# Performance work log

Hardware: AMD Instinct MI355X
Metric: run time of the kernel (lower is better)

The kernel has to match this reference:

```python
import jax, jax.numpy as jnp
import numpy as np

FS = 44100.0
TWO_PI = 2.0 * np.pi


def setup_inputs() -> dict:
    key = jax.random.key(0)
    ks = jax.random.split(key, 12)
    B, T, H, NF, NB = 4, 64000, 96, 4, 8
    f0 = jax.random.uniform(ks[0], (B, T, 1), minval=100.0, maxval=400.0)
    amplitudes = jax.random.uniform(ks[1], (B, T, H))
    vibrato_rate = 5.0 + jax.random.uniform(ks[2], (B, T, 1))
    vibrato_depth = 0.2 * jax.random.uniform(ks[3], (B, T, 1))
    ff = jnp.array([800.0, 1150.0, 2900.0, 3900.0], dtype=jnp.float32)
    fb = jnp.array([80.0, 90.0, 120.0, 130.0], dtype=jnp.float32)
    fg = jnp.array([1.0, 0.5, 0.25, 0.1], dtype=jnp.float32)
    formant_freqs = ff[None, None] * (0.9 + 0.2 * jax.random.uniform(ks[4], (B, T, NF)))
    formant_bandwidths = fb[None, None] * (0.9 + 0.2 * jax.random.uniform(ks[5], (B, T, NF)))
    formant_gains = fg[None, None] * (0.9 + 0.2 * jax.random.uniform(ks[6], (B, T, NF)))
    glottal_open_quotient = 0.5 + 0.4 * jax.random.uniform(ks[7], (B, T, 1))
    phase_coherence = jax.random.uniform(ks[8], (B, T, 1))
    breathiness = 0.3 * jax.random.uniform(ks[9], (B, T, 1))
    breath_spectral_shape = jax.random.uniform(ks[10], (B, T, NB))
    initial_phase = jnp.zeros((B, 1, 1), dtype=jnp.float32)
    return dict(f0=f0, amplitudes=amplitudes, vibrato_rate=vibrato_rate,
                vibrato_depth=vibrato_depth, formant_freqs=formant_freqs,
                formant_bandwidths=formant_bandwidths, formant_gains=formant_gains,
                glottal_open_quotient=glottal_open_quotient,
                phase_coherence=phase_coherence, breathiness=breathiness,
                breath_spectral_shape=breath_spectral_shape, initial_phase=initial_phase)


def _breath_noise(noise, spectral_weights):
    # noise: [B,T]; spectral_weights: [B,n_bands] (mid frame) -> normalized shaped noise [B,T]
    B, T = noise.shape
    n_bands = spectral_weights.shape[1]
    shaped = jnp.zeros_like(noise)
    for i in range(n_bands):  # small fixed band loop (structurally distinct kernel sizes)
        smooth = 2.0 ** (i / 2.0)
        ksz = max(3, int(128 / smooth))
        if ksz % 2 == 0:
            ksz += 1
        g = np.exp(-np.arange(-(ksz // 2), ksz // 2 + 1) ** 2 / (2.0 * (ksz / 6.0) ** 2))
        kern = jnp.asarray(g / g.sum(), dtype=jnp.float32)
        smoothed = jax.lax.conv_general_dilated(
            noise[:, None, :], kern[None, None, :], (1,), 'SAME')[:, 0, :]
        shaped = shaped + smoothed * spectral_weights[:, i:i + 1]
    mean = shaped.mean(axis=1, keepdims=True)
    std = shaped.std(axis=1, ddof=1, keepdims=True) + 1e-8
    return (shaped - mean) / std


def _forward(f0, amplitudes, vibrato_rate, vibrato_depth, formant_freqs,
             formant_bandwidths, formant_gains, glottal_open_quotient,
             phase_coherence, breathiness, breath_spectral_shape, initial_phase, noise):
    B, T, H = amplitudes.shape
    fs = FS
    # --- vibrato ---
    t = (jnp.arange(T, dtype=jnp.float32) / fs)[None, :, None]
    vib_factor = 2.0 ** (vibrato_depth / 12.0)
    vib_mult = jnp.exp(jnp.sin(TWO_PI * vibrato_rate * t) * jnp.log(vib_factor))
    f0_vib = jnp.where(f0 > 0, f0 * vib_mult, f0)  # B,T,1
    # --- per-harmonic phases via cumulative fundamental phase ---
    fund_phase = jnp.cumsum(TWO_PI * f0_vib / fs, axis=1) + initial_phase  # B,T,1
    n = jnp.arange(1, H + 1, dtype=jnp.float32)  # harmonic numbers
    phases = fund_phase * n  # B,T,H
    # --- phase coherence: blend higher harmonics toward n * fundamental ---
    coherent = fund_phase * n[1:]
    blended = phase_coherence * coherent + (1.0 - phase_coherence) * phases[:, :, 1:]
    phases = jnp.concatenate([phases[:, :, :1], blended], axis=2)
    # --- remove above Nyquist ---
    amp = jnp.where(f0_vib * n < fs / 2.0, amplitudes, jnp.zeros_like(amplitudes))
    # --- glottal flow model ---
    norm_phase = jnp.mod(phases, TWO_PI) / TWO_PI
    oq = glottal_open_quotient
    half_pi = jnp.float32(np.pi / 2.0)
    rising = jnp.sin(norm_phase / oq * half_pi) ** 2
    falling = jnp.cos((norm_phase - oq) / (1.0 - oq) * half_pi) ** 2
    flow = jnp.where(norm_phase < oq, rising, falling) - 0.5
    signal = jnp.sum(flow * amp, axis=-1)  # B,T
    # --- formant filter (mid-frame params, vectorized over batch & formants) ---
    mid = T // 2
    freqs = jnp.fft.rfftfreq(T, d=1.0 / fs).astype(jnp.float32)  # [F]
    fmid = formant_freqs[:, mid][:, :, None]       # B,NF,1
    bwmid = formant_bandwidths[:, mid][:, :, None]
    gmid = formant_gains[:, mid][:, :, None]
    resp = (gmid / (1.0 + ((freqs[None, None, :] - fmid) / (bwmid / 2.0)) ** 2)).sum(1)  # B,F
    filtered = jnp.fft.irfft(jnp.fft.rfft(signal) * resp, n=T)  # B,T
    # --- breath noise mix ---
    breath = _breath_noise(noise, breath_spectral_shape[:, mid])  # B,T
    br = breathiness[:, :, 0]
    out = filtered * (1.0 - br) + breath * br
    final_phase = jnp.mod(fund_phase[:, -1:, :], TWO_PI)  # B,1,1
    return out, final_phase


def reference(f0, amplitudes, vibrato_rate, vibrato_depth, formant_freqs,
              formant_bandwidths, formant_gains, glottal_open_quotient,
              phase_coherence, breathiness, breath_spectral_shape, initial_phase):
    B, T = f0.shape[0], f0.shape[1]
    noise = jax.random.normal(jax.random.key(42), (B, T), dtype=jnp.float32)
    return _forward(f0, amplitudes, vibrato_rate, vibrato_depth, formant_freqs,
                    formant_bandwidths, formant_gains, glottal_open_quotient,
                    phase_coherence, breathiness, breath_spectral_shape,
                    initial_phase, noise)
```

## Files before the change

kernel.cpp:

```cpp
#include <hip/hip_runtime.h>
#include <math.h>
#include <stdint.h>

#define B_ 4
#define T_ 64000
#define H_ 96
#define NCH 1000
#define TT_ 64
#define TWO_PI_D 6.283185307179586

typedef float2 cplx;
__device__ __forceinline__ cplx cadd(cplx a, cplx b){ return make_float2(a.x+b.x, a.y+b.y); }
__device__ __forceinline__ cplx csub(cplx a, cplx b){ return make_float2(a.x-b.x, a.y-b.y); }
__device__ __forceinline__ cplx cmul(cplx a, cplx b){ return make_float2(a.x*b.x - a.y*b.y, a.x*b.y + a.y*b.x); }

__device__ float  g_dpf[B_*T_];
__device__ unsigned char g_hcnt[B_*T_];
__device__ float  g_signal[B_*T_];
__device__ float  g_shaped[B_*T_];
__device__ float  g_Kcomb[B_][132];
__device__ float2 g_W1[2*512*125];
__device__ float2 g_Z[2*125*512];
__device__ double g_chunksum[B_*NCH];
__device__ double g_stats[B_*2];
__device__ double g_part[B_*250*2];

__device__ __forceinline__ double fsin64(double x){
  double z = x * 0.63661977236758138243;
  double fn = floor(z + 0.5);
  int k = (int)fn;
  const double p1 = 1.57079632673412561417e+00;
  const double p2 = 6.07710050650619224932e-11;
  double r = x - fn*p1;
  r = r - fn*p2;
  double s = r*r;
  double ps = 1.58969099521155010221e-10;
  ps = ps*s - 2.50507602534068634195e-08;
  ps = ps*s + 2.75573137070700676789e-06;
  ps = ps*s - 1.98412698298579493134e-04;
  ps = ps*s + 8.33333333332248946124e-03;
  ps = ps*s - 1.66666666666666324348e-01;
  double sr = r + r*s*ps;
  double pc = -1.13596475577881948265e-11;
  pc = pc*s + 2.08757232129817482790e-09;
  pc = pc*s - 2.75573143513906633035e-07;
  pc = pc*s + 2.48015872894767294178e-05;
  pc = pc*s - 1.38888888888741095749e-03;
  pc = pc*s + 4.16666666666666019037e-02;
  double cr = 1.0 - 0.5*s + s*s*pc;
  int m = k & 3;
  return (m==0) ? sr : (m==1) ? cr : (m==2) ? -sr : -cr;
}

__device__ __forceinline__ double fexp_small(double x){
  double p = 1.9841269841269841e-04;
  p = p*x + 1.3888888888888889e-03;
  p = p*x + 8.3333333333333332e-03;
  p = p*x + 4.1666666666666664e-02;
  p = p*x + 1.6666666666666666e-01;
  p = p*x + 0.5;
  p = p*x + 1.0;
  p = p*x + 1.0;
  return p;
}

__device__ __forceinline__ uint32_t rotl32(uint32_t x, int r){ return (x<<r)|(x>>(32-r)); }

__device__ __forceinline__ uint32_t threefry_bits(uint32_t i){
  uint32_t x0 = 0u, x1 = i;
  const uint32_t ks0 = 0u, ks1 = 42u, ks2 = 0u ^ 42u ^ 0x1BD11BDAu;
  x0 += ks0; x1 += ks1;
  #define TFR(r) { x0 += x1; x1 = rotl32(x1, r); x1 ^= x0; }
  TFR(13) TFR(15) TFR(26) TFR(6)   x0 += ks1; x1 += ks2 + 1u;
  TFR(17) TFR(29) TFR(16) TFR(24)  x0 += ks2; x1 += ks0 + 2u;
  TFR(13) TFR(15) TFR(26) TFR(6)   x0 += ks0; x1 += ks1 + 3u;
  TFR(17) TFR(29) TFR(16) TFR(24)  x0 += ks1; x1 += ks2 + 4u;
  TFR(13) TFR(15) TFR(26) TFR(6)   x0 += ks2; x1 += ks0 + 5u;
  #undef TFR
  return x0 ^ x1;
}

__device__ __forceinline__ float bits_to_normal(uint32_t bits){
  uint32_t mbits = (bits >> 9) | 0x3F800000u;
  float f = __uint_as_float(mbits) - 1.0f;
  const float lo = -0.99999994f;
  float x = f * 2.0f + lo;
  x = fmaxf(lo, x);
  float w = -log1pf(-x*x);
  float p;
  if (w < 5.0f){
    w -= 2.5f;
    p = 2.81022636e-08f;
    p = fmaf(p, w, 3.43273939e-07f);
    p = fmaf(p, w, -3.5233877e-06f);
    p = fmaf(p, w, -4.39150654e-06f);
    p = fmaf(p, w, 0.00021858087f);
    p = fmaf(p, w, -0.00125372503f);
    p = fmaf(p, w, -0.00417768164f);
    p = fmaf(p, w, 0.246640727f);
    p = fmaf(p, w, 1.50140941f);
  } else {
    w = sqrtf(w) - 3.0f;
    p = -0.000200214257f;
    p = fmaf(p, w, 0.000100950558f);
    p = fmaf(p, w, 0.00134934322f);
    p = fmaf(p, w, -0.00367342844f);
    p = fmaf(p, w, 0.00573950773f);
    p = fmaf(p, w, -0.0076224613f);
    p = fmaf(p, w, 0.00943887047f);
    p = fmaf(p, w, 1.00167406f);
    p = fmaf(p, w, 2.83297682f);
  }
  return 1.4142135623730951f * (p * x);
}

__constant__ int KSZc[8] = {129,91,65,45,33,23,17,11};

__global__ __launch_bounds__(256) void k_phase(const float* __restrict__ bss,
                                               const float* __restrict__ f0,
                                               const float* __restrict__ vr,
                                               const float* __restrict__ vd){
  int b = blockIdx.x / 250, c = blockIdx.x % 250;
  int t0 = c*256, tid = threadIdx.x;
  if (c == 0){
    __shared__ float wn[8];
    {
      int i = tid >> 5, l32 = tid & 31;
      int ksz = KSZc[i];
      float sig = (float)ksz / 6.0f;
      float inv2s2 = 1.0f/(2.0f*sig*sig);
      int ctr = ksz>>1;
      float s = 0.f;
      for (int j = l32; j < ksz; j += 32){
        float d = (float)(j - ctr);
        s += expf(-d*d*inv2s2);
      }
      #pragma unroll
      for (int o=1;o<32;o<<=1) s += __shfl_xor(s, o);
      if (l32 == 0) wn[i] = bss[((size_t)b*T_ + T_/2)*8 + i] / s;
    }
    __syncthreads();
    if (tid < 129){
      int tau = tid - 64;
      float acc = 0.f;
      #pragma unroll
      for (int i=0;i<8;i++){
        int ksz = KSZc[i]; int hw = ksz>>1;
        if (tau >= -hw && tau <= hw){
          float sig = (float)ksz/6.0f;
          float inv2s2 = 1.0f/(2.0f*sig*sig);
          acc += expf(-(float)(tau*tau)*inv2s2) * wn[i];
        }
      }
      g_Kcomb[b][tid] = acc;
    }
  }
  int t = t0 + tid;
  int idx = b*T_ + t;
  double tt = (double)t * 2.2675736961451248e-05;
  double argd = TWO_PI_D * (double)vr[idx] * tt;
  double argr = argd - TWO_PI_D * floor(argd * 0.15915494309189535);
  float svf = __sinf((float)argr);
  double lm = (double)vd[idx] * 0.057762265046662105;
  double vm = fexp_small((double)svf * lm);
  double f0s = (double)f0[idx];
  double f0v = (f0s > 0.0) ? f0s * vm : f0s;
  int cnt;
  if (f0v <= 0.0) cnt = 96;
  else {
    int n = (int)(22050.0f / (float)f0v);
    if (!((double)n * f0v < 22050.0)) n--;
    if ((double)(n+1) * f0v < 22050.0) n++;
    double dlo = 22050.0 - (double)n * f0v;
    double dhi = (double)(n+1) * f0v - 22050.0;
    if (dlo < 0.01 || dhi < 0.01){
      double sv_d = fsin64(argd);
      double vm_d = fexp_small(sv_d * lm);
      double f0x = f0s * vm_d;
      int n2 = (int)(22050.0f / (float)f0x);
      if (!((double)n2 * f0x < 22050.0)) n2--;
      if ((double)(n2+1) * f0x < 22050.0) n2++;
      n = n2;
      f0v = f0x;
    }
    cnt = (n < 0) ? 0 : ((n > 96) ? 96 : n);
  }
  g_hcnt[idx] = (unsigned char)cnt;
  double v = f0v * 1.4247585730565955e-04;
  g_dpf[idx] = (float)v;
  int lane = tid & 63, wid = tid >> 6;
  for (int o=1;o<64;o<<=1) v += __shfl_down(v, o);
  if (lane == 0) g_chunksum[b*NCH + c*4 + wid] = v;
}

__global__ __launch_bounds__(256) void k_synth(const float* __restrict__ amps,
                                               const float* __restrict__ goq,
                                               const float* __restrict__ iph,
                                               float* __restrict__ out_final){
  __shared__ float sh_ns[384];
  __shared__ float sh_kl[132];
  __shared__ float sh_ph[TT_];
  __shared__ double sh_red[8];
  int bid = blockIdx.x;
  int tid = threadIdx.x;
  if ((bid % 5) == 4){
    int bb = bid / 5;
    int b = bb / 250, c = bb % 250;
    int t0 = c * 256;
    for (int k = tid; k < 384; k += 256){
      int t = t0 - 64 + k;
      float nv = 0.f;
      if (t >= 0 && t < T_) nv = bits_to_normal(threefry_bits((uint32_t)(b*T_ + t)));
      sh_ns[k] = nv;
    }
    for (int k = tid; k < 129; k += 256) sh_kl[k] = g_Kcomb[b][k];
    __syncthreads();
    float acc = 0.f;
    for (int j = 0; j < 129; j++) acc = fmaf(sh_ns[tid + j], sh_kl[j], acc);
    g_shaped[b*T_ + t0 + tid] = acc;
    double xx = (double)acc;
    double s1 = xx, s2 = xx*xx;
    for (int o=1;o<64;o<<=1){ s1 += __shfl_down(s1,o); s2 += __shfl_down(s2,o); }
    int lane = tid&63, wid = tid>>6;
    if (lane==0){ sh_red[wid] = s1; sh_red[4+wid] = s2; }
    __syncthreads();
    if (tid==0){
      g_part[(b*250+c)*2]   = sh_red[0]+sh_red[1]+sh_red[2]+sh_red[3];
      g_part[(b*250+c)*2+1] = sh_red[4]+sh_red[5]+sh_red[6]+sh_red[7];
    }
  } else {
    int sb = bid - bid/5;
    int b = sb / NCH, c = sb % NCH;
    int t0 = c * TT_;
    int tl = tid >> 2, part = tid & 3;
    const float4* Ar = (const float4*)(amps + ((size_t)b*T_ + t0 + tl)*H_ + part*24);
    float4 a0 = Ar[0], a1 = Ar[1], a2 = Ar[2], a3 = Ar[3], a4 = Ar[4], a5 = Ar[5];
    int idx = b*T_ + t0 + tl;
    int hc = (int)g_hcnt[idx];
    float oq = goq[idx];
    if (tid < 64){
      double s = 0.0;
      for (int ch = tid; ch < c; ch += 64) s += g_chunksum[b*NCH + ch];
      for (int o=1;o<64;o<<=1) s += __shfl_xor(s, o);
      double base = s + (double)iph[b];
      int idq = b*T_ + t0 + tid;
      double v = (double)g_dpf[idq];
      for (int o=1;o<64;o<<=1){ double u = __shfl_up(v, o); if (tid >= o) v += u; }
      sh_ph[tid] = (float)fmod(base + v, TWO_PI_D);
      if (c == NCH-1 && tid == 63) out_final[b] = (float)fmod(base + v, TWO_PI_D);
    }
    __syncthreads();
    float r = sh_ph[tl];
    float k1 = 3.14159265358979f / oq;
    float k2 = 3.14159265358979f / (1.0f - oq);
    float offA = 3.14159265358979f;
    float offB = -oq * k2;
    float r0 = r * 0.15915494309189535f;
    int hbase = part*24;
    float sum = 0.f;
    float av[24] = {a0.x,a0.y,a0.z,a0.w, a1.x,a1.y,a1.z,a1.w, a2.x,a2.y,a2.z,a2.w,
                    a3.x,a3.y,a3.z,a3.w, a4.x,a4.y,a4.z,a4.w, a5.x,a5.y,a5.z,a5.w};
    #pragma unroll
    for (int e=0;e<24;e++){
      int h = hbase + e;
      float amp = (h < hc) ? av[e] : 0.0f;
      float nn = (float)(h+1);
      float fr = nn * r0;
      fr = fr - floorf(fr);
      bool ris = fr < oq;
      float kk  = ris ? k1 : k2;
      float off = ris ? offA : offB;
      float cv = __cosf(fmaf(fr, kk, off));
      sum = fmaf(cv, amp, sum);
    }
    sum += __shfl_xor(sum, 1);
    sum += __shfl_xor(sum, 2);
    if (part == 0) g_signal[idx] = 0.5f * sum;
  }
}

template<int SGN>
__device__ __forceinline__ float2* fft512_r4(float2* bufA, float2* bufB, int tid){
  float2* src = bufA; float2* dst = bufB;
  #pragma unroll
  for (int st=0; st<4; st++){
    const int s = 1<<(2*st);
    const int n = 512>>(2*st);
    const int m = n>>2;
    if (tid < 128){
      int p = tid / s;
      int q = tid - p*s;
      float2 a0 = src[q + s*p];
      float2 a1 = src[q + s*(p+m)];
      float2 a2 = src[q + s*(p+2*m)];
      float2 a3 = src[q + s*(p+3*m)];
      float2 t0 = cadd(a0,a2), t1 = csub(a0,a2);
      float2 t2 = cadd(a1,a3), t3 = csub(a1,a3);
      float2 it3 = make_float2(-(float)SGN*t3.y, (float)SGN*t3.x);
      float2 r0 = cadd(t0,t2);
      float2 r1 = cadd(t1,it3);
      float2 r2 = csub(t0,t2);
      float2 r3 = csub(t1,it3);
      float ba = (float)SGN * ((float)(2.0*M_PI)/(float)n) * (float)p;
      dst[q + s*(4*p+0)] = r0;
      float sw,cw;
      __sincosf(ba, &sw, &cw);
      dst[q + s*(4*p+1)] = cmul(make_float2(cw,sw), r1);
      __sincosf(2.f*ba, &sw, &cw);
      dst[q + s*(4*p+2)] = cmul(make_float2(cw,sw), r2);
      __sincosf(3.f*ba, &sw, &cw);
      dst[q + s*(4*p+3)] = cmul(make_float2(cw,sw), r3);
    }
    __syncthreads();
    float2* tp = src; src = dst; dst = tp;
  }
  {
    float2 a = src[tid];
    float2 bb = src[tid+256];
    dst[tid]     = cadd(a,bb);
    dst[tid+256] = csub(a,bb);
    __syncthreads();
    float2* tp = src; src = dst; dst = tp;
  }
  return src;
}

__device__ __forceinline__ cplx w5k(int k, float sgn){
  const float C[5] = {1.f, 0.30901699f, -0.80901699f, -0.80901699f, 0.30901699f};
  const float S[5] = {0.f, 0.95105652f, 0.58778525f, -0.58778525f, -0.95105652f};
  return make_float2(C[k], sgn*S[k]);
}

template<int SGN>
__device__ __forceinline__ float2* fft125_rows(float2* bufA, float2* bufB, int tid){
  float2* src = bufA; float2* dst = bufB;
  #pragma unroll
  for (int st=0; st<3; st++){
    const int s = (st==0)?1:((st==1)?5:25);
    const int n = (st==0)?125:((st==1)?25:5);
    const int m = n/5;
    if (tid < 200){
      int row = tid/25, w = tid - row*25;
      int p = w/s, q = w - p*s;
      int base = row*125 + q;
      float2 a0 = src[base + s*p];
      float2 a1 = src[base + s*(p+m)];
      float2 a2 = src[base + s*(p+2*m)];
      float2 a3 = src[base + s*(p+3*m)];
      float2 a4 = src[base + s*(p+4*m)];
      #pragma unroll
      for (int r2=0;r2<5;r2++){
        float2 acc = a0;
        acc = cadd(acc, cmul(a1, w5k((1*r2)%5, (float)SGN)));
        acc = cadd(acc, cmul(a2, w5k((2*r2)%5, (float)SGN)));
        acc = cadd(acc, cmul(a3, w5k((3*r2)%5, (float)SGN)));
        acc = cadd(acc, cmul(a4, w5k((4*r2)%5, (float)SGN)));
        float ang = (float)SGN * ((float)(2.0*M_PI)/(float)n) * (float)(p*r2);
        float sw,cw; __sincosf(ang,&sw,&cw);
        dst[base + s*(5*p+r2)] = cmul(make_float2(cw,sw), acc);
      }
    }
    __syncthreads();
    float2* tp = src; src = dst; dst = tp;
  }
  return src;
}

__global__ __launch_bounds__(256) void k_fft512_fwd(){
  int p = blockIdx.x / 125, n1 = blockIdx.x % 125;
  int tid = threadIdx.x;
  __shared__ float2 bufA[512];
  __shared__ float2 bufB[512];
  const float* sa = g_signal + (size_t)(2*p)*T_;
  const float* sb = g_signal + (size_t)(2*p+1)*T_;
  for (int i=tid;i<512;i+=256) bufA[i] = make_float2(sa[n1 + 125*i], sb[n1 + 125*i]);
  __syncthreads();
  float2* res = fft512_r4<-1>(bufA, bufB, tid);
  for (int i=tid;i<512;i+=256){
    float ang = -(float)(2.0*M_PI/64000.0) * (float)(n1*i);
    float sw,cw; __sincosf(ang,&sw,&cw);
    g_W1[((size_t)p*512 + i)*125 + n1] = cmul(make_float2(cw,sw), res[i]);
  }
  if (blockIdx.x < B_){
    int b = blockIdx.x;
    double s1=0.0, s2=0.0;
    if (tid < 250){ s1 = g_part[(b*250+tid)*2]; s2 = g_part[(b*250+tid)*2+1]; }
    for (int o=1;o<64;o<<=1){ s1 += __shfl_down(s1,o); s2 += __shfl_down(s2,o); }
    __shared__ double a1[4], a2[4];
    int lane = tid&63, wid = tid>>6;
    if (lane==0){ a1[wid]=s1; a2[wid]=s2; }
    __syncthreads();
    if (tid==0){
      double S1=a1[0]+a1[1]+a1[2]+a1[3], S2=a2[0]+a2[1]+a2[2]+a2[3];
      double mean = S1 / (double)T_;
      double var = (S2 - (double)T_*mean*mean) / (double)(T_-1);
      if (var < 0.0) var = 0.0;
      double rstd = 1.0/(sqrt(var) + 1e-8);
      g_stats[b*2] = mean; g_stats[b*2+1] = rstd;
    }
  }
}

__global__ __launch_bounds__(256) void k_fft125_mid(const float* __restrict__ ffq,
                                                    const float* __restrict__ fbw,
                                                    const float* __restrict__ fgn){
  int p = blockIdx.x / 64;
  int j = blockIdx.x % 64;
  int tid = threadIdx.x;
  __shared__ float2 bufA[1000];
  __shared__ float2 bufB[1000];
  int k2r[8];
  #pragma unroll
  for (int l=0;l<8;l++){
    int k2;
    if (l < 4) k2 = 4*j + l;
    else if (j==0 && l==4) k2 = 256;
    else k2 = 512 - 4*j - (l-4);
    k2r[l] = k2;
  }
  for (int i=tid;i<1000;i+=256){
    int l = i/125, n1 = i - l*125;
    bufA[i] = g_W1[((size_t)p*512 + k2r[l])*125 + n1];
  }
  float fca[4], bwa[4], ga[4], fcb[4], bwb[4], gb[4];
  int ba = 2*p, bb = 2*p+1;
  #pragma unroll
  for (int q=0;q<4;q++){
    size_t ia = ((size_t)ba*T_ + T_/2)*4 + q;
    size_t ib = ((size_t)bb*T_ + T_/2)*4 + q;
    fca[q]=ffq[ia]; bwa[q]=fbw[ia]; ga[q]=fgn[ia];
    fcb[q]=ffq[ib]; bwb[q]=fbw[ib]; gb[q]=fgn[ib];
  }
  __syncthreads();
  float2* X = fft125_rows<-1>(bufA, bufB, tid);
  float2* Y = (X == bufA) ? bufB : bufA;
  for (int i=tid;i<1000;i+=256){
    int l = i/125, k1 = i - l*125;
    int k2 = k2r[l];
    int lm = ((j==0) && (l==0 || l==4)) ? l : (l^4);
    int k1m = (k2 == 0) ? ((k1==0)?0:(125-k1)) : (124-k1);
    float2 Z1 = X[l*125 + k1];
    float2 Z2 = X[lm*125 + k1m];
    float xax = 0.5f*(Z1.x + Z2.x), xay = 0.5f*(Z1.y - Z2.y);
    float xbx = 0.5f*(Z1.y + Z2.y), xby = -0.5f*(Z1.x - Z2.x);
    int f = k2 + 512*k1;
    int fi = (f <= 32000) ? f : (64000 - f);
    float freq = (float)fi * 0.6890625f;
    float ra = 0.f, rb = 0.f;
    #pragma unroll
    for (int q=0;q<4;q++){
      float da = (freq - fca[q]) / (bwa[q]*0.5f);
      ra += ga[q] / (1.0f + da*da);
      float db = (freq - fcb[q]) / (bwb[q]*0.5f);
      rb += gb[q] / (1.0f + db*db);
    }
    float yax = ra*xax, yay = ra*xay;
    float ybx = rb*xbx, yby = rb*xby;
    Y[i] = make_float2(yax - yby, yay + ybx);
  }
  __syncthreads();
  float2* res2 = fft125_rows<1>(Y, X, tid);
  for (int i=tid;i<1000;i+=256){
    int l = i/125, n1 = i - l*125;
    int k2 = k2r[l];
    float ang = (float)(2.0*M_PI/64000.0) * (float)(n1*k2);
    float sw,cw; __sincosf(ang,&sw,&cw);
    g_Z[((size_t)p*125 + n1)*512 + k2] = cmul(make_float2(cw,sw), res2[i]);
  }
}

__global__ __launch_bounds__(256) void k_fft512_inv(const float* __restrict__ brth,
                                                    float* __restrict__ outp){
  int p = blockIdx.x / 125, n1 = blockIdx.x % 125;
  int tid = threadIdx.x;
  __shared__ float2 bufA[512];
  __shared__ float2 bufB[512];
  const float2* gin = g_Z + ((size_t)p*125 + n1)*512;
  for (int i=tid;i<512;i+=256) bufA[i] = gin[i];
  __syncthreads();
  float2* res = fft512_r4<1>(bufA, bufB, tid);
  int ba = 2*p, bb = 2*p+1;
  float mean_a = (float)g_stats[ba*2], rstd_a = (float)g_stats[ba*2+1];
  float mean_b = (float)g_stats[bb*2], rstd_b = (float)g_stats[bb*2+1];
  for (int i=tid;i<512;i+=256){
    int t = n1 + 125*i;
    float2 v = res[i];
    {
      int idx = ba*T_ + t;
      float filt = v.x * (1.0f/64000.0f);
      float br = brth[idx];
      float breath = (g_shaped[idx] - mean_a) * rstd_a;
      outp[idx] = filt*(1.0f - br) + breath*br;
    }
    {
      int idx = bb*T_ + t;
      float filt = v.y * (1.0f/64000.0f);
      float br = brth[idx];
      float breath = (g_shaped[idx] - mean_b) * rstd_b;
      outp[idx] = filt*(1.0f - br) + breath*br;
    }
  }
}

extern "C" void kernel_launch(void* const* d_in, const int* in_sizes, int n_in,
                              void* d_out, int out_size, void* d_ws, size_t ws_size,
                              hipStream_t stream){
  (void)in_sizes; (void)n_in; (void)out_size; (void)d_ws; (void)ws_size;
  const float* f0   = (const float*)d_in[0];
  const float* amps = (const float*)d_in[1];
  const float* vr   = (const float*)d_in[2];
  const float* vd   = (const float*)d_in[3];
  const float* ffq  = (const float*)d_in[4];
  const float* fbw  = (const float*)d_in[5];
  const float* fgn  = (const float*)d_in[6];
  const float* goq  = (const float*)d_in[7];
  const float* brth = (const float*)d_in[9];
  const float* bss  = (const float*)d_in[10];
  const float* iph  = (const float*)d_in[11];
  float* out = (float*)d_out;
  float* out_final = out + (size_t)B_*T_;

  k_phase<<<B_*250,256,0,stream>>>(bss, f0, vr, vd);
  k_synth<<<5000,256,0,stream>>>(amps, goq, iph, out_final);
  k_fft512_fwd<<<250,256,0,stream>>>();
  k_fft125_mid<<<128,256,0,stream>>>(ffq, fbw, fgn);
  k_fft512_inv<<<250,256,0,stream>>>(brth, out);
}
```

Baseline: 56.02 us.

## Process four synth chunks per block with double-buffered amplitude prefetch

Each synthesis block now handles four consecutive 64-sample chunks instead of one. It prefetches the next chunk's amplitude rows into registers while computing the current chunk, and ping-pongs phase values in shared memory. The prefix sum over earlier chunk sums is done once per four chunks, and later chunk bases are carried forward incrementally. Block interleaving with the noise-shaping blocks changes from 4:1 to 1:1, and the grid shrinks to 2000 blocks. The trade-off is higher register pressure from holding two sets of amplitudes, fewer blocks to spread across the GPU, and extra block-wide syncs.

```diff
diff --git a/kernel.cpp b/kernel.cpp
--- a/kernel.cpp
+++ b/kernel.cpp
@@ -193,18 +193,49 @@
   if (lane == 0) g_chunksum[b*NCH + c*4 + wid] = v;
 }
 
+__device__ __forceinline__ void compute_tile(float4 a0,float4 a1,float4 a2,float4 a3,float4 a4,float4 a5,
+                                             const float* phbuf, int hc, float oq, int idx,
+                                             int tl, int part){
+  float r = phbuf[tl];
+  float k1 = 3.14159265358979f / oq;
+  float k2 = 3.14159265358979f / (1.0f - oq);
+  float offA = 3.14159265358979f;
+  float offB = -oq * k2;
+  float r0 = r * 0.15915494309189535f;
+  int hbase = part*24;
+  float sum = 0.f;
+  float av[24] = {a0.x,a0.y,a0.z,a0.w, a1.x,a1.y,a1.z,a1.w, a2.x,a2.y,a2.z,a2.w,
+                  a3.x,a3.y,a3.z,a3.w, a4.x,a4.y,a4.z,a4.w, a5.x,a5.y,a5.z,a5.w};
+  #pragma unroll
+  for (int e=0;e<24;e++){
+    int h = hbase + e;
+    float amp = (h < hc) ? av[e] : 0.0f;
+    float nn = (float)(h+1);
+    float fr = nn * r0;
+    fr = fr - floorf(fr);
+    bool ris = fr < oq;
+    float kk  = ris ? k1 : k2;
+    float off = ris ? offA : offB;
+    float cv = __cosf(fmaf(fr, kk, off));
+    sum = fmaf(cv, amp, sum);
+  }
+  sum += __shfl_xor(sum, 1);
+  sum += __shfl_xor(sum, 2);
+  if (part == 0) g_signal[idx] = 0.5f * sum;
+}
+
 __global__ __launch_bounds__(256) void k_synth(const float* __restrict__ amps,
                                                const float* __restrict__ goq,
                                                const float* __restrict__ iph,
                                                float* __restrict__ out_final){
   __shared__ float sh_ns[384];
   __shared__ float sh_kl[132];
-  __shared__ float sh_ph[TT_];
+  __shared__ float sh_ph[2][TT_];
   __shared__ double sh_red[8];
   int bid = blockIdx.x;
   int tid = threadIdx.x;
-  if ((bid % 5) == 4){
-    int bb = bid / 5;
+  if (bid & 1){
+    int bb = bid >> 1;
     int b = bb / 250, c = bb % 250;
     int t0 = c * 256;
     for (int k = tid; k < 384; k += 256){
@@ -229,53 +260,64 @@
       g_part[(b*250+c)*2+1] = sh_red[4]+sh_red[5]+sh_red[6]+sh_red[7];
     }
   } else {
-    int sb = bid - bid/5;
-    int b = sb / NCH, c = sb % NCH;
-    int t0 = c * TT_;
+    int sb = bid >> 1;
+    int b = sb / 250;
+    int cbase = (sb % 250) * 4;
     int tl = tid >> 2, part = tid & 3;
-    const float4* Ar = (const float4*)(amps + ((size_t)b*T_ + t0 + tl)*H_ + part*24);
-    float4 a0 = Ar[0], a1 = Ar[1], a2 = Ar[2], a3 = Ar[3], a4 = Ar[4], a5 = Ar[5];
-    int idx = b*T_ + t0 + tl;
-    int hc = (int)g_hcnt[idx];
-    float oq = goq[idx];
+    size_t rb = (size_t)b*T_;
+    int t00 = (cbase+0)*TT_, t01 = (cbase+1)*TT_, t02 = (cbase+2)*TT_, t03 = (cbase+3)*TT_;
+    const float4* P0 = (const float4*)(amps + (rb + t00 + tl)*H_ + part*24);
+    float4 A0=P0[0],A1=P0[1],A2=P0[2],A3=P0[3],A4=P0[4],A5=P0[5];
+    int idx0 = b*T_ + t00 + tl; int hc0 = (int)g_hcnt[idx0]; float oq0 = goq[idx0];
+    double base = 0.0;
     if (tid < 64){
       double s = 0.0;
-      for (int ch = tid; ch < c; ch += 64) s += g_chunksum[b*NCH + ch];
+      for (int ch = tid; ch < cbase; ch += 64) s += g_chunksum[b*NCH + ch];
       for (int o=1;o<64;o<<=1) s += __shfl_xor(s, o);
-      double base = s + (double)iph[b];
-      int idq = b*T_ + t0 + tid;
-      double v = (double)g_dpf[idq];
-      for (int o=1;o<64;o<<=1){ double u = __shfl_up(v, o); if (tid >= o) v += u; }
-      sh_ph[tid] = (float)fmod(base + v, TWO_PI_D);
-      if (c == NCH-1 && tid == 63) out_final[b] = (float)fmod(base + v, TWO_PI_D);
-    }
-    __syncthreads();
-    float r = sh_ph[tl];
-    float k1 = 3.14159265358979f / oq;
-    float k2 = 3.14159265358979f / (1.0f - oq);
-    float offA = 3.14159265358979f;
-    float offB = -oq * k2;
-    float r0 = r * 0.15915494309189535f;
-    int hbase = part*24;
-    float sum = 0.f;
-    float av[24] = {a0.x,a0.y,a0.z,a0.w, a1.x,a1.y,a1.z,a1.w, a2.x,a2.y,a2.z,a2.w,
-                    a3.x,a3.y,a3.z,a3.w, a4.x,a4.y,a4.z,a4.w, a5.x,a5.y,a5.z,a5.w};
-    #pragma unroll
-    for (int e=0;e<24;e++){
-      int h = hbase + e;
-      float amp = (h < hc) ? av[e] : 0.0f;
-      float nn = (float)(h+1);
-      float fr = nn * r0;
-      fr = fr - floorf(fr);
-      bool ris = fr < oq;
-      float kk  = ris ? k1 : k2;
-      float off = ris ? offA : offB;
-      float cv = __cosf(fmaf(fr, kk, off));
-      sum = fmaf(cv, amp, sum);
-    }
-    sum += __shfl_xor(sum, 1);
-    sum += __shfl_xor(sum, 2);
-    if (part == 0) g_signal[idx] = 0.5f * sum;
+      base = s + (double)iph[b];
+    }
+    if (tid < 64){
+      double v = (double)g_dpf[b*T_ + t00 + tid];
+      for (int o=1;o<64;o<<=1){ double u = __shfl_up(v,o); if (tid>=o) v += u; }
+      sh_ph[0][tid] = (float)fmod(base + v, TWO_PI_D);
+      base += g_chunksum[b*NCH + cbase + 0];
+    }
+    __syncthreads();
+    const float4* P1 = (const float4*)(amps + (rb + t01 + tl)*H_ + part*24);
+    float4 B0=P1[0],B1=P1[1],B2=P1[2],B3=P1[3],B4=P1[4],B5=P1[5];
+    int idx1 = b*T_ + t01 + tl; int hc1 = (int)g_hcnt[idx1]; float oq1 = goq[idx1];
+    compute_tile(A0,A1,A2,A3,A4,A5, sh_ph[0], hc0, oq0, idx0, tl, part);
+    if (tid < 64){
+      double v = (double)g_dpf[b*T_ + t01 + tid];
+      for (int o=1;o<64;o<<=1){ double u = __shfl_up(v,o); if (tid>=o) v += u; }
+      sh_ph[1][tid] = (float)fmod(base + v, TWO_PI_D);
+      base += g_chunksum[b*NCH + cbase + 1];
+    }
+    __syncthreads();
+    const float4* P2 = (const float4*)(amps + (rb + t02 + tl)*H_ + part*24);
+    A0=P2[0];A1=P2[1];A2=P2[2];A3=P2[3];A4=P2[4];A5=P2[5];
+    int idx2 = b*T_ + t02 + tl; int hc2 = (int)g_hcnt[idx2]; float oq2 = goq[idx2];
+    compute_tile(B0,B1,B2,B3,B4,B5, sh_ph[1], hc1, oq1, idx1, tl, part);
+    if (tid < 64){
+      double v = (double)g_dpf[b*T_ + t02 + tid];
+      for (int o=1;o<64;o<<=1){ double u = __shfl_up(v,o); if (tid>=o) v += u; }
+      sh_ph[0][tid] = (float)fmod(base + v, TWO_PI_D);
+      base += g_chunksum[b*NCH + cbase + 2];
+    }
+    __syncthreads();
+    const float4* P3 = (const float4*)(amps + (rb + t03 + tl)*H_ + part*24);
+    B0=P3[0];B1=P3[1];B2=P3[2];B3=P3[3];B4=P3[4];B5=P3[5];
+    int idx3 = b*T_ + t03 + tl; int hc3 = (int)g_hcnt[idx3]; float oq3 = goq[idx3];
+    compute_tile(A0,A1,A2,A3,A4,A5, sh_ph[0], hc2, oq2, idx2, tl, part);
+    if (tid < 64){
+      double v = (double)g_dpf[b*T_ + t03 + tid];
+      for (int o=1;o<64;o<<=1){ double u = __shfl_up(v,o); if (tid>=o) v += u; }
+      double ful = base + v;
+      sh_ph[1][tid] = (float)fmod(ful, TWO_PI_D);
+      if (cbase + 3 == NCH-1 && tid == 63) out_final[b] = (float)fmod(ful, TWO_PI_D);
+    }
+    __syncthreads();
+    compute_tile(B0,B1,B2,B3,B4,B5, sh_ph[1], hc3, oq3, idx3, tl, part);
   }
 }
 
@@ -521,7 +563,7 @@
   float* out_final = out + (size_t)B_*T_;
 
   k_phase<<<B_*250,256,0,stream>>>(bss, f0, vr, vd);
-  k_synth<<<5000,256,0,stream>>>(amps, goq, iph, out_final);
+  k_synth<<<2000,256,0,stream>>>(amps, goq, iph, out_final);
   k_fft512_fwd<<<250,256,0,stream>>>();
   k_fft125_mid<<<128,256,0,stream>>>(ffq, fbw, fgn);
   k_fft512_inv<<<250,256,0,stream>>>(brth, out);
```

After: 69.23 us. 23.6% more time.
